# Kernel tuning notes

Hardware: AMD Instinct MI355X
Metric: run time of the kernel (lower is better)

The kernel has to match this reference:

```python
import jax, jax.numpy as jnp
import numpy as np

B, T, DIM, H = 2, 2048, 2048, 16
HD = DIM // H  # 128
ROPE_BASE = 10000.0


def _rope_angles(seq_len, head_dim, offset=0, dtype=jnp.float32):
    inv_freq = 1.0 / (ROPE_BASE ** (jnp.arange(0, head_dim, 2, dtype=dtype) / head_dim))
    pos = jnp.arange(offset, offset + seq_len, dtype=dtype)
    ang = pos[:, None] * inv_freq[None, :]              # [T, HD/2]
    ang = jnp.concatenate([ang, ang], axis=-1)          # [T, HD]
    return jnp.cos(ang), jnp.sin(ang)


def _rotate_half(x):
    x1, x2 = jnp.split(x, 2, axis=-1)
    return jnp.concatenate([-x2, x1], axis=-1)


def setup_inputs() -> dict:
    key = jax.random.key(0)
    ks = jax.random.split(key, 5)
    s = 0.02
    return {
        "x": jax.random.normal(ks[0], (B, T, DIM), dtype=jnp.float32),
        "Wq": jax.random.normal(ks[1], (DIM, DIM), dtype=jnp.float32) * s,
        "Wk": jax.random.normal(ks[2], (DIM, HD), dtype=jnp.float32) * s,
        "Wv": jax.random.normal(ks[3], (DIM, HD), dtype=jnp.float32) * s,
        "Wo": jax.random.normal(ks[4], (DIM, DIM), dtype=jnp.float32) * s,
    }


def reference(x, Wq, Wk, Wv, Wo):
    # q: [B, H, T, HD]; k, v: single shared head [B, T, HD]
    q = (x @ Wq).reshape(B, T, H, HD).transpose(0, 2, 1, 3)
    k = x @ Wk
    v = x @ Wv

    # RoPE (offset=0, no kv cache)
    cos, sin = _rope_angles(T, HD, 0, x.dtype)
    q = q * cos[None, None] + _rotate_half(q) * sin[None, None]
    k = k * cos[None] + _rotate_half(k) * sin[None]

    present_k = k[:, None]  # [B, 1, T, HD]
    present_v = v[:, None]

    # MQA attention: broadcast shared KV head via einsum (no materialized expand)
    scale = 1.0 / jnp.sqrt(jnp.asarray(HD, x.dtype))
    scores = jnp.einsum('bhqd,bkd->bhqk', q, k) * scale  # [B, H, T, T]
    causal = jnp.tril(jnp.ones((T, T), dtype=bool))
    scores = jnp.where(causal[None, None], scores, jnp.finfo(scores.dtype).min)
    attn = jax.nn.softmax(scores, axis=-1)
    out = jnp.einsum('bhqk,bkd->bhqd', attn, v)          # [B, H, T, HD]
    out = out.transpose(0, 2, 1, 3).reshape(B, T, DIM) @ Wo
    return (out, present_k, present_v)
```

## Files before the change

### kernel.cpp

```cpp
#include <hip/hip_runtime.h>


typedef __attribute__((ext_vector_type(8))) short short8;
typedef __attribute__((ext_vector_type(4))) float float4v;
typedef __attribute__((ext_vector_type(4))) unsigned short ushort4v;

#define LOG2E 1.4426950408889634f
#define ATT_SCALE 0.08838834764831845f
#define RLOG 0.20762050593046014f

__device__ __forceinline__ float bf2f(ushort u) {
    union { unsigned u; float f; } v; v.u = ((unsigned)u) << 16; return v.f;
}
__device__ __forceinline__ ushort f2bf(float f) {
    union { float f; unsigned u; } v; v.f = f;
    return (ushort)((v.u + 0x7FFF + ((v.u >> 16) & 1)) >> 16);
}
__device__ __forceinline__ ushort f2bf_fast(float f) {
    union { float f; unsigned u; } v; v.f = f;
    return (ushort)((v.u + 0x8000u) >> 16);
}
__device__ __forceinline__ float4v mfma16(short8 a, short8 b, float4v c) {
    return __builtin_amdgcn_mfma_f32_16x16x32_bf16(a, b, c, 0, 0, 0);
}
__device__ __forceinline__ void gl_lds16(const ushort* g, ushort* l) {
    __builtin_amdgcn_global_load_lds(
        (const __attribute__((address_space(1))) unsigned int*)g,
        (__attribute__((address_space(3))) unsigned int*)l, 16, 0, 0);
}

__global__ __launch_bounds__(256) void prep(const float* __restrict__ x,
                                            ushort* __restrict__ x_bf,
                                            float* __restrict__ tbl) {
    int bid = blockIdx.x;
    if (bid < 512) {
        int idx = bid * 256 + threadIdx.x;
        int d = idx & 63, t = idx >> 6;
        float inv = exp2f(-(float)d * RLOG);
        float s, c;
        sincosf((float)t * inv, &s, &c);
        tbl[idx * 2] = c;  tbl[idx * 2 + 1] = s;
    } else {
        int i = ((bid - 512) * 256 + threadIdx.x) * 4;
        float4v v = *(const float4v*)&x[i];
        ushort4v u;
        #pragma unroll
        for (int r = 0; r < 4; ++r) u[r] = f2bf(v[r]);
        *(ushort4v*)&x_bf[i] = u;
    }
}

__global__ __launch_bounds__(256) void transpose_cvt(const float* __restrict__ in,
                                                     ushort* __restrict__ out,
                                                     int M, int N) {
    __shared__ ushort tile[32][33];
    int cb = blockIdx.x * 32, rb = blockIdx.y * 32;
    int x = threadIdx.x, y0 = threadIdx.y;
    #pragma unroll
    for (int i = 0; i < 32; i += 8)
        tile[y0 + i][x] = f2bf(in[(long)(rb + y0 + i) * N + cb + x]);
    __syncthreads();
    #pragma unroll
    for (int i = 0; i < 32; i += 8)
        out[(long)(cb + y0 + i) * M + rb + x] = tile[x][y0 + i];
}

__global__ __launch_bounds__(256) void transpose_bf16(const ushort* __restrict__ in,
                                                      ushort* __restrict__ out,
                                                      int M, int N) {
    __shared__ ushort tile[32][33];
    int cb = blockIdx.x * 32, rb = blockIdx.y * 32;
    int x = threadIdx.x, y0 = threadIdx.y;
    #pragma unroll
    for (int i = 0; i < 32; i += 8)
        tile[y0 + i][x] = in[(long)(rb + y0 + i) * N + cb + x];
    __syncthreads();
    #pragma unroll
    for (int i = 0; i < 32; i += 8)
        out[(long)(cb + y0 + i) * M + rb + x] = tile[x][y0 + i];
}

__global__ __launch_bounds__(256) void gemm_qkv(const ushort* __restrict__ A,
                                                const ushort* __restrict__ W,
                                                ushort* __restrict__ Cq,
                                                ushort* __restrict__ Ck,
                                                ushort* __restrict__ Cv) {
    constexpr int BM = 128, BN = 128, K = 2048;
    constexpr int SM = 64, SN = 64, MT = 4, NT = 4;
    __shared__ ushort As[BM * 32];
    __shared__ ushort Bs[BN * 32];
    const int m0 = blockIdx.y * BM, n0 = blockIdx.x * BN;
    const int tid = threadIdx.x;
    const int wave = tid >> 6, lane = tid & 63, l15 = lane & 15, quad = lane >> 4;
    const int wr = wave >> 1, wc = wave & 1;

    float4v acc[MT][NT] = {};

    for (int k0 = 0; k0 < K; k0 += 32) {
        __syncthreads();
        #pragma unroll
        for (int p = 0; p < 2; ++p) {
            int lin = (p * 4 + wave) * 64 + lane;
            int row = lin >> 2, c8 = (lin & 3) * 8;
            gl_lds16(&A[(long)(m0 + row) * K + k0 + c8], &As[(p * 4 + wave) * 512]);
        }
        #pragma unroll
        for (int p = 0; p < 2; ++p) {
            int lin = (p * 4 + wave) * 64 + lane;
            int row = lin >> 2, c8 = (lin & 3) * 8;
            gl_lds16(&W[(long)(n0 + row) * K + k0 + c8], &Bs[(p * 4 + wave) * 512]);
        }
        __syncthreads();

        short8 a[MT], b[NT];
        #pragma unroll
        for (int mt = 0; mt < MT; ++mt)
            a[mt] = *(const short8*)&As[(wr * SM + mt * 16 + l15) * 32 + quad * 8];
        #pragma unroll
        for (int nt = 0; nt < NT; ++nt)
            b[nt] = *(const short8*)&Bs[(wc * SN + nt * 16 + l15) * 32 + quad * 8];
        #pragma unroll
        for (int mt = 0; mt < MT; ++mt)
            #pragma unroll
            for (int nt = 0; nt < NT; ++nt)
                acc[mt][nt] = mfma16(a[mt], b[nt], acc[mt][nt]);
    }
    ushort* C;  int Nc, coff;
    if (n0 < 2048)      { C = Cq; Nc = 2048; coff = n0; }
    else if (n0 < 2176) { C = Ck; Nc = 128;  coff = n0 - 2048; }
    else                { C = Cv; Nc = 128;  coff = n0 - 2176; }
    #pragma unroll
    for (int mt = 0; mt < MT; ++mt)
        #pragma unroll
        for (int nt = 0; nt < NT; ++nt)
            #pragma unroll
            for (int r = 0; r < 4; ++r) {
                int row = m0 + wr * SM + mt * 16 + quad * 4 + r;
                int col = coff + wc * SN + nt * 16 + l15;
                C[(long)row * Nc + col] = f2bf(acc[mt][nt][r]);
            }
}

__global__ __launch_bounds__(256) void gemm_out(const ushort* __restrict__ A,
                                                const ushort* __restrict__ W,
                                                float* __restrict__ C) {
    constexpr int BM = 128, BN = 128, K = 2048, N = 2048;
    constexpr int SM = 64, SN = 64, MT = 4, NT = 4;
    __shared__ ushort As[BM * 32];
    __shared__ ushort Bs[BN * 32];
    const int m0 = blockIdx.y * BM, n0 = blockIdx.x * BN;
    const int tid = threadIdx.x;
    const int wave = tid >> 6, lane = tid & 63, l15 = lane & 15, quad = lane >> 4;
    const int wr = wave >> 1, wc = wave & 1;

    float4v acc[MT][NT] = {};

    for (int k0 = 0; k0 < K; k0 += 32) {
        __syncthreads();
        #pragma unroll
        for (int p = 0; p < 2; ++p) {
            int lin = (p * 4 + wave) * 64 + lane;
            int row = lin >> 2, c8 = (lin & 3) * 8;
            gl_lds16(&A[(long)(m0 + row) * K + k0 + c8], &As[(p * 4 + wave) * 512]);
        }
        #pragma unroll
        for (int p = 0; p < 2; ++p) {
            int lin = (p * 4 + wave) * 64 + lane;
            int row = lin >> 2, c8 = (lin & 3) * 8;
            gl_lds16(&W[(long)(n0 + row) * K + k0 + c8], &Bs[(p * 4 + wave) * 512]);
        }
        __syncthreads();

        short8 a[MT], b[NT];
        #pragma unroll
        for (int mt = 0; mt < MT; ++mt)
            a[mt] = *(const short8*)&As[(wr * SM + mt * 16 + l15) * 32 + quad * 8];
        #pragma unroll
        for (int nt = 0; nt < NT; ++nt)
            b[nt] = *(const short8*)&Bs[(wc * SN + nt * 16 + l15) * 32 + quad * 8];
        #pragma unroll
        for (int mt = 0; mt < MT; ++mt)
            #pragma unroll
            for (int nt = 0; nt < NT; ++nt)
                acc[mt][nt] = mfma16(a[mt], b[nt], acc[mt][nt]);
    }
    #pragma unroll
    for (int mt = 0; mt < MT; ++mt)
        #pragma unroll
        for (int nt = 0; nt < NT; ++nt)
            #pragma unroll
            for (int r = 0; r < 4; ++r) {
                int row = m0 + wr * SM + mt * 16 + quad * 4 + r;
                int col = n0 + wc * SN + nt * 16 + l15;
                C[(long)row * N + col] = acc[mt][nt][r];
            }
}

template<int BM, int BN>
__global__ __launch_bounds__(256) void gemm_bt_f32(const float* __restrict__ A32,
                                                   const ushort* __restrict__ B0,
                                                   const ushort* __restrict__ B1,
                                                   ushort* __restrict__ C0,
                                                   ushort* __restrict__ C1,
                                                   int M, int N, int K) {
    constexpr int SM = BM / 2, SN = BN / 2;
    constexpr int MT = SM / 16, NT = SN / 16;
    constexpr int LDK = 40;
    __shared__ ushort As[BM * LDK];
    __shared__ ushort Bs[BN * LDK];
    const ushort* Bm = blockIdx.z ? B1 : B0;
    ushort* C = blockIdx.z ? C1 : C0;
    const int m0 = blockIdx.y * BM, n0 = blockIdx.x * BN;
    const int tid = threadIdx.x;
    const int wave = tid >> 6, lane = tid & 63, l15 = lane & 15, quad = lane >> 4;
    const int wr = wave >> 1, wc = wave & 1;
    float4v acc[MT][NT] = {};
    for (int k0 = 0; k0 < K; k0 += 32) {
        #pragma unroll
        for (int p = 0; p < (BM * 32) / (256 * 4); ++p) {
            int lin = p * 256 + tid;
            int row = lin >> 3, c4 = (lin & 7) * 4;
            float4v v = *(const float4v*)&A32[(long)(m0 + row) * K + k0 + c4];
            ushort4v u;
            #pragma unroll
            for (int i = 0; i < 4; ++i) u[i] = f2bf(v[i]);
            *(ushort4v*)&As[row * LDK + c4] = u;
        }
        #pragma unroll
        for (int p = 0; p < (BN * 4) / 256; ++p) {
            int lin = p * 256 + tid;
            int row = lin >> 2, c8 = (lin & 3) * 8;
            *(short8*)&Bs[row * LDK + c8] =
                *(const short8*)&Bm[(long)(n0 + row) * K + k0 + c8];
        }
        __syncthreads();
        short8 a[MT], b[NT];
        #pragma unroll
        for (int mt = 0; mt < MT; ++mt)
            a[mt] = *(const short8*)&As[(wr * SM + mt * 16 + l15) * LDK + quad * 8];
        #pragma unroll
        for (int nt = 0; nt < NT; ++nt)
            b[nt] = *(const short8*)&Bs[(wc * SN + nt * 16 + l15) * LDK + quad * 8];
        #pragma unroll
        for (int mt = 0; mt < MT; ++mt)
            #pragma unroll
            for (int nt = 0; nt < NT; ++nt)
                acc[mt][nt] = mfma16(a[mt], b[nt], acc[mt][nt]);
        __syncthreads();
    }
    #pragma unroll
    for (int mt = 0; mt < MT; ++mt)
        #pragma unroll
        for (int nt = 0; nt < NT; ++nt)
            #pragma unroll
            for (int r = 0; r < 4; ++r) {
                int row = m0 + wr * SM + mt * 16 + quad * 4 + r;
                int col = n0 + wc * SN + nt * 16 + l15;
                C[(long)row * N + col] = f2bf(acc[mt][nt][r]);
            }
}
__global__ __launch_bounds__(256) void gemm_out_f32A(const float* __restrict__ A32,
                                                     const ushort* __restrict__ W,
                                                     float* __restrict__ C) {
}

__global__ __launch_bounds__(256) void rope_k_present(ushort* __restrict__ Kw,
                                                      const ushort* __restrict__ Vw,
                                                      const float* __restrict__ tbl,
                                                      float* __restrict__ outK,
                                                      float* __restrict__ outV) {
    int idx = blockIdx.x * 256 + threadIdx.x;
    int d = idx & 63;
    int row = idx >> 6;
    int t = row & 2047;
    float c = tbl[(t * 64 + d) * 2], s = tbl[(t * 64 + d) * 2 + 1];
    long base = (long)row * 128 + d;
    float k1 = bf2f(Kw[base]), k2 = bf2f(Kw[base + 64]);
    float r1 = k1 * c - k2 * s, r2 = k2 * c + k1 * s;
    Kw[base] = f2bf(r1);  Kw[base + 64] = f2bf(r2);
    outK[base] = r1;      outK[base + 64] = r2;
    outV[base] = bf2f(Vw[base]); outV[base + 64] = bf2f(Vw[base + 64]);
}

__global__ __launch_bounds__(256, 4) void flash_mqa5(ushort* __restrict__ Q,
                                                     const ushort* __restrict__ Kg,
                                                     const ushort* __restrict__ Vt,
                                                     const float* __restrict__ tbl) {
    constexpr int T = 2048, DIM = 2048;
    constexpr float SCL2 = ATT_SCALE * LOG2E;
    constexpr int LDK = 136, LDP = 40;
    __shared__ ushort Ks[32 * LDK];
    __shared__ ushort Vs[128 * LDP];
    __shared__ ushort Ps[4][16 * LDP];
    const int j = blockIdx.x;
    const int b = j >> 9, u = j & 511;
    const int f = u >> 8, r0 = u & 255;
    const int h = r0 & 15, q4 = r0 >> 4;
    const int qb = f ? 31 - q4 : q4;
    const int qbase = qb * 64;
    const int tid = threadIdx.x;
    const int wave = tid >> 6, lane = tid & 63, l15 = lane & 15, quad = lane >> 4;
    const int tq = qbase + wave * 16 + l15;
    const int qminw = qbase + wave * 16, qmaxw = qminw + 15;

    short8 qf[4];
    ushort* qp = Q + (long)(b * T + tq) * DIM + h * 128 + quad * 8;
    #pragma unroll
    for (int kc = 0; kc < 4; ++kc) qf[kc] = *(const short8*)(qp + kc * 32);
    #pragma unroll
    for (int kc = 0; kc < 2; ++kc) {
        float ang[16];
        const float4v* tb = (const float4v*)(tbl + ((long)tq * 64 + kc * 32 + quad * 8) * 2);
        *(float4v*)&ang[0]  = tb[0];
        *(float4v*)&ang[4]  = tb[1];
        *(float4v*)&ang[8]  = tb[2];
        *(float4v*)&ang[12] = tb[3];
        #pragma unroll
        for (int jj = 0; jj < 8; ++jj) {
            float cs = ang[2 * jj] * SCL2, sn = ang[2 * jj + 1] * SCL2;
            float x1 = bf2f((ushort)qf[kc][jj]);
            float x2 = bf2f((ushort)qf[kc + 2][jj]);
            qf[kc][jj]     = (short)f2bf(x1 * cs - x2 * sn);
            qf[kc + 2][jj] = (short)f2bf(x2 * cs + x1 * sn);
        }
    }

    float4v o[8] = {};
    float l_part = 0.f;

    const ushort* kb_ptr = Kg + (long)b * T * 128;
    const ushort* vb_ptr = Vt + (long)b * T;
    const int nkb = 2 * (qb + 1);

    const int krow = tid >> 3, kseg = tid & 7;
    const int vd = tid >> 1, vseg = tid & 1;
    short8 kreg[2], vreg[2];
    #pragma unroll
    for (int c = 0; c < 2; ++c) {
        kreg[c] = *(const short8*)&kb_ptr[(long)krow * 128 + kseg * 16 + c * 8];
        vreg[c] = *(const short8*)&vb_ptr[(long)vd * 4096 + vseg * 16 + c * 8];
    }

    for (int kb = 0; kb < nkb; ++kb) {
        const int k0 = kb * 32;
        __syncthreads();
        #pragma unroll
        for (int c = 0; c < 2; ++c) {
            *(short8*)&Ks[krow * LDK + kseg * 16 + c * 8] = kreg[c];
            *(short8*)&Vs[vd * LDP + vseg * 16 + c * 8] = vreg[c];
        }
        __syncthreads();
        if (kb + 1 < nkb) {
            const int kn = k0 + 32;
            #pragma unroll
            for (int c = 0; c < 2; ++c) {
                kreg[c] = *(const short8*)&kb_ptr[(long)(kn + krow) * 128 + kseg * 16 + c * 8];
                vreg[c] = *(const short8*)&vb_ptr[(long)vd * 4096 + kn + vseg * 16 + c * 8];
            }
        }
        if (k0 > qmaxw) continue;

        float4v st[2] = {};
        #pragma unroll
        for (int sub = 0; sub < 2; ++sub)
            #pragma unroll
            for (int kc = 0; kc < 4; ++kc) {
                short8 kf = *(const short8*)&Ks[(sub * 16 + l15) * LDK + kc * 32 + quad * 8];
                st[sub] = mfma16(kf, qf[kc], st[sub]);
            }

        const bool diag = (k0 + 31 > qminw);
        ushort* Pw = &Ps[wave][0];
        #pragma unroll
        for (int sub = 0; sub < 2; ++sub) {
            ushort4v pv4;
            #pragma unroll
            for (int r = 0; r < 4; ++r) {
                float zz = st[sub][r];
                if (diag) {
                    int key = k0 + sub * 16 + quad * 4 + r;
                    zz = (key <= tq) ? zz : -INFINITY;
                }
                float pv = exp2f(zz);
                l_part += pv;
                pv4[r] = f2bf_fast(pv);
            }
            *(ushort4v*)&Pw[l15 * LDP + sub * 16 + quad * 4] = pv4;
        }

        short8 pf = *(const short8*)&Pw[l15 * LDP + quad * 8];
        #pragma unroll
        for (int nt = 0; nt < 8; ++nt) {
            short8 vf = *(const short8*)&Vs[(nt * 16 + l15) * LDP + quad * 8];
            o[nt] = mfma16(vf, pf, o[nt]);
        }
    }

    float rs = l_part;
    rs += __shfl_xor(rs, 16);
    rs += __shfl_xor(rs, 32);
    float inv_l = 1.0f / rs;
    ushort* dst = Q + (long)(b * T + tq) * DIM + h * 128;
    #pragma unroll
    for (int nt = 0; nt < 8; ++nt) {
        ushort4v v;
        #pragma unroll
        for (int r = 0; r < 4; ++r) v[r] = f2bf(o[nt][r] * inv_l);
        *(ushort4v*)&dst[nt * 16 + quad * 4] = v;
    }
}

extern "C" void kernel_launch(void* const* d_in, const int* in_sizes, int n_in,
                              void* d_out, int out_size, void* d_ws, size_t ws_size,
                              hipStream_t stream) {
    const float* x  = (const float*)d_in[0];
    const float* Wq = (const float*)d_in[1];
    const float* Wk = (const float*)d_in[2];
    const float* Wv = (const float*)d_in[3];
    const float* Wo = (const float*)d_in[4];
    float* out = (float*)d_out;

    char* ws = (char*)d_ws;
    const bool precast = ws_size >= (46u << 20);
    dim3 tb(32, 8);

    if (precast) {
        ushort* x_bf  = (ushort*)(ws);
        ushort* q_bf  = (ushort*)(ws + (16u << 20));
        ushort* WT    = (ushort*)(ws + (32u << 20));
        ushort* k_bf  = (ushort*)(ws + (42u << 20));
        ushort* v_bf  = (ushort*)(ws + (43u << 20));
        ushort* vt_bf = (ushort*)(ws + (44u << 20));
        float*  ropet = (float*)(ws + (45u << 20));

        prep<<<8704, 256, 0, stream>>>(x, x_bf, ropet);
        transpose_cvt<<<dim3(64, 64), tb, 0, stream>>>(Wq, WT, 2048, 2048);
        transpose_cvt<<<dim3(4, 64),  tb, 0, stream>>>(Wk, WT + (long)2048 * 2048, 2048, 128);
        transpose_cvt<<<dim3(4, 64),  tb, 0, stream>>>(Wv, WT + (long)2176 * 2048, 2048, 128);

        gemm_qkv<<<dim3(18, 32), 256, 0, stream>>>(x_bf, WT, q_bf, k_bf, v_bf);

        rope_k_present<<<1024, 256, 0, stream>>>(k_bf, v_bf, ropet,
                                                 out + 8388608, out + 8912896);
        transpose_bf16<<<dim3(4, 128), tb, 0, stream>>>(v_bf, vt_bf, 4096, 128);

        flash_mqa5<<<1024, 256, 0, stream>>>(q_bf, k_bf, vt_bf, ropet);

        transpose_cvt<<<dim3(64, 64), tb, 0, stream>>>(Wo, WT, 2048, 2048);
        gemm_out<<<dim3(16, 32), 256, 0, stream>>>(q_bf, WT, out);
    } else {
        ushort* q_bf  = (ushort*)(ws);
        ushort* WT    = (ushort*)(ws + (16u << 20));
        ushort* k_bf  = (ushort*)(ws + (26u << 20));
        ushort* v_bf  = (ushort*)(ws + (27u << 20));
        ushort* vt_bf = (ushort*)(ws + (28u << 20));
        float*  ropet = (float*)(ws + (29u << 20));
        ushort* WkT = WT + (long)2048 * 2048;
        ushort* WvT = WT + (long)2176 * 2048;

        prep<<<512, 256, 0, stream>>>(x, nullptr, ropet);
        transpose_cvt<<<dim3(64, 64), tb, 0, stream>>>(Wq, WT, 2048, 2048);
        transpose_cvt<<<dim3(4, 64),  tb, 0, stream>>>(Wk, WkT, 2048, 128);
        transpose_cvt<<<dim3(4, 64),  tb, 0, stream>>>(Wv, WvT, 2048, 128);

        gemm_bt_f32<128,128><<<dim3(16, 32, 1), 256, 0, stream>>>(
            x, WT, WT, q_bf, q_bf, 4096, 2048, 2048);
        gemm_bt_f32<64,64><<<dim3(2, 64, 2), 256, 0, stream>>>(
            x, WkT, WvT, k_bf, v_bf, 4096, 128, 2048);

        rope_k_present<<<1024, 256, 0, stream>>>(k_bf, v_bf, ropet,
                                                 out + 8388608, out + 8912896);
        transpose_bf16<<<dim3(4, 128), tb, 0, stream>>>(v_bf, vt_bf, 4096, 128);

        flash_mqa5<<<1024, 256, 0, stream>>>(q_bf, k_bf, vt_bf, ropet);

        transpose_cvt<<<dim3(64, 64), tb, 0, stream>>>(Wo, WT, 2048, 2048);
        gemm_out<<<dim3(16, 32), 256, 0, stream>>>(q_bf, WT, out);
    }
}
```

Baseline: 306.2 us.

## Merge prep/transpose launches and widen flash attention key blocks to 64

Folds the x cast, RoPE table and the Wq/Wk/Wv transposes into one grid-partitioned launch. Likewise folds K RoPE plus present writes, the V transpose and the Wo transpose into a second single launch, cutting the launch count and the tail gaps between kernels. The flash MQA kernel now processes 64-key blocks instead of 32, halving barrier and loop iterations, and interleaves causal-heavy and causal-light query blocks in adjacent block IDs. It also uses packed bf16 conversions and lowers the occupancy hint from 4 to 3; the larger LDS and register footprint may reduce occupancy.

```diff
diff --git a/kernel.cpp b/kernel.cpp
--- a/kernel.cpp
+++ b/kernel.cpp
@@ -1,9 +1,11 @@
 #include <hip/hip_runtime.h>
+#include <hip/hip_bf16.h>
 
 
 typedef __attribute__((ext_vector_type(8))) short short8;
 typedef __attribute__((ext_vector_type(4))) float float4v;
 typedef __attribute__((ext_vector_type(4))) unsigned short ushort4v;
+typedef __attribute__((ext_vector_type(2))) unsigned int uint2v;
 
 #define LOG2E 1.4426950408889634f
 #define ATT_SCALE 0.08838834764831845f
@@ -16,9 +18,10 @@
     union { float f; unsigned u; } v; v.f = f;
     return (ushort)((v.u + 0x7FFF + ((v.u >> 16) & 1)) >> 16);
 }
-__device__ __forceinline__ ushort f2bf_fast(float f) {
-    union { float f; unsigned u; } v; v.f = f;
-    return (ushort)((v.u + 0x8000u) >> 16);
+__device__ __forceinline__ unsigned pk2bf(float a, float b) {
+    union { __hip_bfloat162 h; unsigned u; } v;
+    v.h = __float22bfloat162_rn(make_float2(a, b));
+    return v.u;
 }
 __device__ __forceinline__ float4v mfma16(short8 a, short8 b, float4v c) {
     return __builtin_amdgcn_mfma_f32_16x16x32_bf16(a, b, c, 0, 0, 0);
@@ -29,55 +32,97 @@
         (__attribute__((address_space(3))) unsigned int*)l, 16, 0, 0);
 }
 
-__global__ __launch_bounds__(256) void prep(const float* __restrict__ x,
-                                            ushort* __restrict__ x_bf,
-                                            float* __restrict__ tbl) {
-    int bid = blockIdx.x;
+__global__ __launch_bounds__(256) void prep_all(const float* __restrict__ x,
+                                                ushort* __restrict__ x_bf,
+                                                const float* __restrict__ Wq,
+                                                const float* __restrict__ Wk,
+                                                const float* __restrict__ Wv,
+                                                ushort* __restrict__ WT,
+                                                float* __restrict__ tbl) {
+    __shared__ ushort tile[32][33];
+    const int bid = blockIdx.x, tid = threadIdx.x;
     if (bid < 512) {
-        int idx = bid * 256 + threadIdx.x;
+        int idx = bid * 256 + tid;
         int d = idx & 63, t = idx >> 6;
         float inv = exp2f(-(float)d * RLOG);
         float s, c;
         sincosf((float)t * inv, &s, &c);
         tbl[idx * 2] = c;  tbl[idx * 2 + 1] = s;
-    } else {
-        int i = ((bid - 512) * 256 + threadIdx.x) * 4;
-        float4v v = *(const float4v*)&x[i];
-        ushort4v u;
-        #pragma unroll
-        for (int r = 0; r < 4; ++r) u[r] = f2bf(v[r]);
-        *(ushort4v*)&x_bf[i] = u;
-    }
-}
-
-__global__ __launch_bounds__(256) void transpose_cvt(const float* __restrict__ in,
-                                                     ushort* __restrict__ out,
-                                                     int M, int N) {
+        return;
+    }
+    if (bid < 8704) {
+        if (x_bf) {
+            int i = ((bid - 512) * 256 + tid) * 4;
+            float4v v = *(const float4v*)&x[i];
+            ushort4v u;
+            #pragma unroll
+            for (int r = 0; r < 4; ++r) u[r] = f2bf(v[r]);
+            *(ushort4v*)&x_bf[i] = u;
+        }
+        return;
+    }
+    const float* in;  ushort* out;  int N, tb;
+    if (bid < 12800)      { tb = bid - 8704;  in = Wq; out = WT;                        N = 2048; }
+    else if (bid < 13056) { tb = bid - 12800; in = Wk; out = WT + (long)2048 * 2048;    N = 128; }
+    else                  { tb = bid - 13056; in = Wv; out = WT + (long)2176 * 2048;    N = 128; }
+    const int gx = N / 32;
+    int cb = (tb % gx) * 32, rb = (tb / gx) * 32;
+    int xx = tid & 31, y0 = tid >> 5;
+    #pragma unroll
+    for (int i = 0; i < 32; i += 8)
+        tile[y0 + i][xx] = f2bf(in[(long)(rb + y0 + i) * N + cb + xx]);
+    __syncthreads();
+    #pragma unroll
+    for (int i = 0; i < 32; i += 8)
+        out[(long)(cb + y0 + i) * 2048 + rb + xx] = tile[xx][y0 + i];
+}
+
+__global__ __launch_bounds__(256) void ropekv_wo(ushort* __restrict__ Kw,
+                                                 const ushort* __restrict__ Vw,
+                                                 ushort* __restrict__ vt_bf,
+                                                 const float* __restrict__ Wo,
+                                                 ushort* __restrict__ WT,
+                                                 const float* __restrict__ tbl,
+                                                 float* __restrict__ outK,
+                                                 float* __restrict__ outV) {
     __shared__ ushort tile[32][33];
-    int cb = blockIdx.x * 32, rb = blockIdx.y * 32;
-    int x = threadIdx.x, y0 = threadIdx.y;
+    const int bid = blockIdx.x, tid = threadIdx.x;
+    if (bid < 1024) {
+        int idx = bid * 256 + tid;
+        int d = idx & 63;
+        int row = idx >> 6;
+        int t = row & 2047;
+        float c = tbl[(t * 64 + d) * 2], s = tbl[(t * 64 + d) * 2 + 1];
+        long base = (long)row * 128 + d;
+        float k1 = bf2f(Kw[base]), k2 = bf2f(Kw[base + 64]);
+        float r1 = k1 * c - k2 * s, r2 = k2 * c + k1 * s;
+        Kw[base] = f2bf(r1);  Kw[base + 64] = f2bf(r2);
+        outK[base] = r1;      outK[base + 64] = r2;
+        outV[base] = bf2f(Vw[base]); outV[base + 64] = bf2f(Vw[base + 64]);
+        return;
+    }
+    int xx = tid & 31, y0 = tid >> 5;
+    if (bid < 1536) {
+        int tb = bid - 1024;
+        int cb = (tb & 3) * 32, rb = (tb >> 2) * 32;
+        #pragma unroll
+        for (int i = 0; i < 32; i += 8)
+            tile[y0 + i][xx] = Vw[(long)(rb + y0 + i) * 128 + cb + xx];
+        __syncthreads();
+        #pragma unroll
+        for (int i = 0; i < 32; i += 8)
+            vt_bf[(long)(cb + y0 + i) * 4096 + rb + xx] = tile[xx][y0 + i];
+        return;
+    }
+    int tb = bid - 1536;
+    int cb = (tb & 63) * 32, rb = (tb >> 6) * 32;
     #pragma unroll
     for (int i = 0; i < 32; i += 8)
-        tile[y0 + i][x] = f2bf(in[(long)(rb + y0 + i) * N + cb + x]);
+        tile[y0 + i][xx] = f2bf(Wo[(long)(rb + y0 + i) * 2048 + cb + xx]);
     __syncthreads();
     #pragma unroll
     for (int i = 0; i < 32; i += 8)
-        out[(long)(cb + y0 + i) * M + rb + x] = tile[x][y0 + i];
-}
-
-__global__ __launch_bounds__(256) void transpose_bf16(const ushort* __restrict__ in,
-                                                      ushort* __restrict__ out,
-                                                      int M, int N) {
-    __shared__ ushort tile[32][33];
-    int cb = blockIdx.x * 32, rb = blockIdx.y * 32;
-    int x = threadIdx.x, y0 = threadIdx.y;
-    #pragma unroll
-    for (int i = 0; i < 32; i += 8)
-        tile[y0 + i][x] = in[(long)(rb + y0 + i) * N + cb + x];
-    __syncthreads();
-    #pragma unroll
-    for (int i = 0; i < 32; i += 8)
-        out[(long)(cb + y0 + i) * M + rb + x] = tile[x][y0 + i];
+        WT[(long)(cb + y0 + i) * 2048 + rb + xx] = tile[xx][y0 + i];
 }
 
 __global__ __launch_bounds__(256) void gemm_qkv(const ushort* __restrict__ A,
@@ -85,11 +130,11 @@
                                                 ushort* __restrict__ Cq,
                                                 ushort* __restrict__ Ck,
                                                 ushort* __restrict__ Cv) {
-    constexpr int BM = 128, BN = 128, K = 2048;
+    constexpr int BM = 128, K = 2048;
     constexpr int SM = 64, SN = 64, MT = 4, NT = 4;
     __shared__ ushort As[BM * 32];
-    __shared__ ushort Bs[BN * 32];
-    const int m0 = blockIdx.y * BM, n0 = blockIdx.x * BN;
+    __shared__ ushort Bs[128 * 32];
+    const int m0 = blockIdx.y * BM, n0 = blockIdx.x * 128;
     const int tid = threadIdx.x;
     const int wave = tid >> 6, lane = tid & 63, l15 = lane & 15, quad = lane >> 4;
     const int wr = wave >> 1, wc = wave & 1;
@@ -144,11 +189,11 @@
 __global__ __launch_bounds__(256) void gemm_out(const ushort* __restrict__ A,
                                                 const ushort* __restrict__ W,
                                                 float* __restrict__ C) {
-    constexpr int BM = 128, BN = 128, K = 2048, N = 2048;
+    constexpr int BM = 128, K = 2048, N = 2048;
     constexpr int SM = 64, SN = 64, MT = 4, NT = 4;
     __shared__ ushort As[BM * 32];
-    __shared__ ushort Bs[BN * 32];
-    const int m0 = blockIdx.y * BM, n0 = blockIdx.x * BN;
+    __shared__ ushort Bs[128 * 32];
+    const int m0 = blockIdx.y * BM, n0 = blockIdx.x * 128;
     const int tid = threadIdx.x;
     const int wave = tid >> 6, lane = tid & 63, l15 = lane & 15, quad = lane >> 4;
     const int wr = wave >> 1, wc = wave & 1;
@@ -259,49 +304,27 @@
                 C[(long)row * N + col] = f2bf(acc[mt][nt][r]);
             }
 }
-__global__ __launch_bounds__(256) void gemm_out_f32A(const float* __restrict__ A32,
-                                                     const ushort* __restrict__ W,
-                                                     float* __restrict__ C) {
-}
-
-__global__ __launch_bounds__(256) void rope_k_present(ushort* __restrict__ Kw,
-                                                      const ushort* __restrict__ Vw,
-                                                      const float* __restrict__ tbl,
-                                                      float* __restrict__ outK,
-                                                      float* __restrict__ outV) {
-    int idx = blockIdx.x * 256 + threadIdx.x;
-    int d = idx & 63;
-    int row = idx >> 6;
-    int t = row & 2047;
-    float c = tbl[(t * 64 + d) * 2], s = tbl[(t * 64 + d) * 2 + 1];
-    long base = (long)row * 128 + d;
-    float k1 = bf2f(Kw[base]), k2 = bf2f(Kw[base + 64]);
-    float r1 = k1 * c - k2 * s, r2 = k2 * c + k1 * s;
-    Kw[base] = f2bf(r1);  Kw[base + 64] = f2bf(r2);
-    outK[base] = r1;      outK[base + 64] = r2;
-    outV[base] = bf2f(Vw[base]); outV[base + 64] = bf2f(Vw[base + 64]);
-}
-
-__global__ __launch_bounds__(256, 4) void flash_mqa5(ushort* __restrict__ Q,
+
+__global__ __launch_bounds__(256, 3) void flash_mqa6(ushort* __restrict__ Q,
                                                      const ushort* __restrict__ Kg,
                                                      const ushort* __restrict__ Vt,
                                                      const float* __restrict__ tbl) {
     constexpr int T = 2048, DIM = 2048;
     constexpr float SCL2 = ATT_SCALE * LOG2E;
-    constexpr int LDK = 136, LDP = 40;
-    __shared__ ushort Ks[32 * LDK];
+    constexpr int LDK = 136, LDP = 72;
+    __shared__ ushort Ks[64 * LDK];
     __shared__ ushort Vs[128 * LDP];
     __shared__ ushort Ps[4][16 * LDP];
     const int j = blockIdx.x;
-    const int b = j >> 9, u = j & 511;
-    const int f = u >> 8, r0 = u & 255;
-    const int h = r0 & 15, q4 = r0 >> 4;
-    const int qb = f ? 31 - q4 : q4;
+    const int b = j >> 9, r0 = j & 511;
+    const int odd = r0 & 1, pr = r0 >> 1;
+    const int h = pr & 15, q4 = pr >> 4;
+    const int qb = odd ? 31 - q4 : q4;
     const int qbase = qb * 64;
     const int tid = threadIdx.x;
     const int wave = tid >> 6, lane = tid & 63, l15 = lane & 15, quad = lane >> 4;
     const int tq = qbase + wave * 16 + l15;
-    const int qminw = qbase + wave * 16, qmaxw = qminw + 15;
+    const int qminw = qbase + wave * 16;
 
     short8 qf[4];
     ushort* qp = Q + (long)(b * T + tq) * DIM + h * 128 + quad * 8;
@@ -330,50 +353,49 @@
 
     const ushort* kb_ptr = Kg + (long)b * T * 128;
     const ushort* vb_ptr = Vt + (long)b * T;
-    const int nkb = 2 * (qb + 1);
-
-    const int krow = tid >> 3, kseg = tid & 7;
+    const int nkb = qb + 1;
+
+    const int krow = tid >> 2, kseg = tid & 3;
     const int vd = tid >> 1, vseg = tid & 1;
-    short8 kreg[2], vreg[2];
-    #pragma unroll
-    for (int c = 0; c < 2; ++c) {
-        kreg[c] = *(const short8*)&kb_ptr[(long)krow * 128 + kseg * 16 + c * 8];
-        vreg[c] = *(const short8*)&vb_ptr[(long)vd * 4096 + vseg * 16 + c * 8];
+    short8 kreg[4], vreg[4];
+    #pragma unroll
+    for (int c = 0; c < 4; ++c) {
+        kreg[c] = *(const short8*)&kb_ptr[(long)krow * 128 + kseg * 32 + c * 8];
+        vreg[c] = *(const short8*)&vb_ptr[(long)vd * 4096 + vseg * 32 + c * 8];
     }
 
     for (int kb = 0; kb < nkb; ++kb) {
-        const int k0 = kb * 32;
-        __syncthreads();
-        #pragma unroll
-        for (int c = 0; c < 2; ++c) {
-            *(short8*)&Ks[krow * LDK + kseg * 16 + c * 8] = kreg[c];
-            *(short8*)&Vs[vd * LDP + vseg * 16 + c * 8] = vreg[c];
+        const int k0 = kb * 64;
+        __syncthreads();
+        #pragma unroll
+        for (int c = 0; c < 4; ++c) {
+            *(short8*)&Ks[krow * LDK + kseg * 32 + c * 8] = kreg[c];
+            *(short8*)&Vs[vd * LDP + vseg * 32 + c * 8] = vreg[c];
         }
         __syncthreads();
         if (kb + 1 < nkb) {
-            const int kn = k0 + 32;
-            #pragma unroll
-            for (int c = 0; c < 2; ++c) {
-                kreg[c] = *(const short8*)&kb_ptr[(long)(kn + krow) * 128 + kseg * 16 + c * 8];
-                vreg[c] = *(const short8*)&vb_ptr[(long)vd * 4096 + kn + vseg * 16 + c * 8];
-            }
-        }
-        if (k0 > qmaxw) continue;
-
-        float4v st[2] = {};
-        #pragma unroll
-        for (int sub = 0; sub < 2; ++sub)
+            const int kn = k0 + 64;
+            #pragma unroll
+            for (int c = 0; c < 4; ++c) {
+                kreg[c] = *(const short8*)&kb_ptr[(long)(kn + krow) * 128 + kseg * 32 + c * 8];
+                vreg[c] = *(const short8*)&vb_ptr[(long)vd * 4096 + kn + vseg * 32 + c * 8];
+            }
+        }
+
+        float4v st[4] = {};
+        #pragma unroll
+        for (int sub = 0; sub < 4; ++sub)
             #pragma unroll
             for (int kc = 0; kc < 4; ++kc) {
                 short8 kf = *(const short8*)&Ks[(sub * 16 + l15) * LDK + kc * 32 + quad * 8];
                 st[sub] = mfma16(kf, qf[kc], st[sub]);
             }
 
-        const bool diag = (k0 + 31 > qminw);
+        const bool diag = (k0 + 63 > qminw);
         ushort* Pw = &Ps[wave][0];
         #pragma unroll
-        for (int sub = 0; sub < 2; ++sub) {
-            ushort4v pv4;
+        for (int sub = 0; sub < 4; ++sub) {
+            float pv[4];
             #pragma unroll
             for (int r = 0; r < 4; ++r) {
                 float zz = st[sub][r];
@@ -381,18 +403,21 @@
                     int key = k0 + sub * 16 + quad * 4 + r;
                     zz = (key <= tq) ? zz : -INFINITY;
                 }
-                float pv = exp2f(zz);
-                l_part += pv;
-                pv4[r] = f2bf_fast(pv);
-            }
-            *(ushort4v*)&Pw[l15 * LDP + sub * 16 + quad * 4] = pv4;
-        }
-
-        short8 pf = *(const short8*)&Pw[l15 * LDP + quad * 8];
-        #pragma unroll
-        for (int nt = 0; nt < 8; ++nt) {
-            short8 vf = *(const short8*)&Vs[(nt * 16 + l15) * LDP + quad * 8];
-            o[nt] = mfma16(vf, pf, o[nt]);
+                pv[r] = exp2f(zz);
+                l_part += pv[r];
+            }
+            uint2v u2 = { pk2bf(pv[0], pv[1]), pk2bf(pv[2], pv[3]) };
+            *(uint2v*)&Pw[l15 * LDP + sub * 16 + quad * 4] = u2;
+        }
+
+        #pragma unroll
+        for (int kc2 = 0; kc2 < 2; ++kc2) {
+            short8 pf = *(const short8*)&Pw[l15 * LDP + kc2 * 32 + quad * 8];
+            #pragma unroll
+            for (int nt = 0; nt < 8; ++nt) {
+                short8 vf = *(const short8*)&Vs[(nt * 16 + l15) * LDP + kc2 * 32 + quad * 8];
+                o[nt] = mfma16(vf, pf, o[nt]);
+            }
         }
     }
 
@@ -403,10 +428,9 @@
     ushort* dst = Q + (long)(b * T + tq) * DIM + h * 128;
     #pragma unroll
     for (int nt = 0; nt < 8; ++nt) {
-        ushort4v v;
-        #pragma unroll
-        for (int r = 0; r < 4; ++r) v[r] = f2bf(o[nt][r] * inv_l);
-        *(ushort4v*)&dst[nt * 16 + quad * 4] = v;
+        uint2v u2 = { pk2bf(o[nt][0] * inv_l, o[nt][1] * inv_l),
+                      pk2bf(o[nt][2] * inv_l, o[nt][3] * inv_l) };
+        *(uint2v*)&dst[nt * 16 + quad * 4] = u2;
     }
 }
 
@@ -422,7 +446,6 @@
 
     char* ws = (char*)d_ws;
     const bool precast = ws_size >= (46u << 20);
-    dim3 tb(32, 8);
 
     if (precast) {
         ushort* x_bf  = (ushort*)(ws);
@@ -433,20 +456,11 @@
         ushort* vt_bf = (ushort*)(ws + (44u << 20));
         float*  ropet = (float*)(ws + (45u << 20));
 
-        prep<<<8704, 256, 0, stream>>>(x, x_bf, ropet);
-        transpose_cvt<<<dim3(64, 64), tb, 0, stream>>>(Wq, WT, 2048, 2048);
-        transpose_cvt<<<dim3(4, 64),  tb, 0, stream>>>(Wk, WT + (long)2048 * 2048, 2048, 128);
-        transpose_cvt<<<dim3(4, 64),  tb, 0, stream>>>(Wv, WT + (long)2176 * 2048, 2048, 128);
-
+        prep_all<<<13312, 256, 0, stream>>>(x, x_bf, Wq, Wk, Wv, WT, ropet);
         gemm_qkv<<<dim3(18, 32), 256, 0, stream>>>(x_bf, WT, q_bf, k_bf, v_bf);
-
-        rope_k_present<<<1024, 256, 0, stream>>>(k_bf, v_bf, ropet,
-                                                 out + 8388608, out + 8912896);
-        transpose_bf16<<<dim3(4, 128), tb, 0, stream>>>(v_bf, vt_bf, 4096, 128);
-
-        flash_mqa5<<<1024, 256, 0, stream>>>(q_bf, k_bf, vt_bf, ropet);
-
-        transpose_cvt<<<dim3(64, 64), tb, 0, stream>>>(Wo, WT, 2048, 2048);
+        ropekv_wo<<<5632, 256, 0, stream>>>(k_bf, v_bf, vt_bf, Wo, WT, ropet,
+                                            out + 8388608, out + 8912896);
+        flash_mqa6<<<1024, 256, 0, stream>>>(q_bf, k_bf, vt_bf, ropet);
         gemm_out<<<dim3(16, 32), 256, 0, stream>>>(q_bf, WT, out);
     } else {
         ushort* q_bf  = (ushort*)(ws);
@@ -458,23 +472,14 @@
         ushort* WkT = WT + (long)2048 * 2048;
         ushort* WvT = WT + (long)2176 * 2048;
 
-        prep<<<512, 256, 0, stream>>>(x, nullptr, ropet);
-        transpose_cvt<<<dim3(64, 64), tb, 0, stream>>>(Wq, WT, 2048, 2048);
-        transpose_cvt<<<dim3(4, 64),  tb, 0, stream>>>(Wk, WkT, 2048, 128);
-        transpose_cvt<<<dim3(4, 64),  tb, 0, stream>>>(Wv, WvT, 2048, 128);
-
+        prep_all<<<13312, 256, 0, stream>>>(x, nullptr, Wq, Wk, Wv, WT, ropet);
         gemm_bt_f32<128,128><<<dim3(16, 32, 1), 256, 0, stream>>>(
             x, WT, WT, q_bf, q_bf, 4096, 2048, 2048);
         gemm_bt_f32<64,64><<<dim3(2, 64, 2), 256, 0, stream>>>(
             x, WkT, WvT, k_bf, v_bf, 4096, 128, 2048);
-
-        rope_k_present<<<1024, 256, 0, stream>>>(k_bf, v_bf, ropet,
-                                                 out + 8388608, out + 8912896);
-        transpose_bf16<<<dim3(4, 128), tb, 0, stream>>>(v_bf, vt_bf, 4096, 128);
-
-        flash_mqa5<<<1024, 256, 0, stream>>>(q_bf, k_bf, vt_bf, ropet);
-
-        transpose_cvt<<<dim3(64, 64), tb, 0, stream>>>(Wo, WT, 2048, 2048);
+        ropekv_wo<<<5632, 256, 0, stream>>>(k_bf, v_bf, vt_bf, Wo, WT, ropet,
+                                            out + 8388608, out + 8912896);
+        flash_mqa6<<<1024, 256, 0, stream>>>(q_bf, k_bf, vt_bf, ropet);
         gemm_out<<<dim3(16, 32), 256, 0, stream>>>(q_bf, WT, out);
     }
 }
```

Measured after the change: 330.4 us. +7.9%, slower.
